# Performance work log

Hardware: AMD Instinct MI355X
Metric: run time of the kernel (lower is better)

Reference implementation:

```python
import jax, jax.numpy as jnp
import numpy as np
import math

EMBED = 1024
HEADS = 16
HEAD_DIM = EMBED // HEADS
B, S = 2, 2048


def setup_inputs() -> dict:
    key = jax.random.key(0)
    ks = jax.random.split(key, 12)
    sc = 1.0 / math.sqrt(EMBED)
    inp = {
        'query': jax.random.normal(ks[0], (B, S, EMBED), jnp.float32),
        'key': jax.random.normal(ks[1], (B, S, EMBED), jnp.float32),
        'values': jax.random.normal(ks[2], (B, S, EMBED), jnp.float32),
        # causal mask, broadcastable to [B, H, S, S]; masked where == 0
        'mask': jnp.tril(jnp.ones((S, S), jnp.int32))[None, None, :, :],
        'Wq': jax.random.normal(ks[3], (EMBED, EMBED), jnp.float32) * sc,
        'bq': jnp.zeros((EMBED,), jnp.float32),
        'Wk': jax.random.normal(ks[4], (EMBED, EMBED), jnp.float32) * sc,
        'bk': jnp.zeros((EMBED,), jnp.float32),
        'Wv': jax.random.normal(ks[5], (EMBED, EMBED), jnp.float32) * sc,
        'bv': jnp.zeros((EMBED,), jnp.float32),
        'Wo': jax.random.normal(ks[6], (EMBED, EMBED), jnp.float32) * sc,
        'bo': jnp.zeros((EMBED,), jnp.float32),
    }
    return inp


def reference(query, key, values, mask, Wq, bq, Wk, bk, Wv, bv, Wo, bo):
    # linear projections (torch Linear: x @ W.T + b)
    q = query @ Wq.T + bq
    k = key @ Wk.T + bk
    v = values @ Wv.T + bv
    b, sq, _ = q.shape
    sk = k.shape[1]
    q = q.reshape(b, sq, HEADS, HEAD_DIM)  # bqhd
    k = k.reshape(b, sk, HEADS, HEAD_DIM)  # bkhd
    v = v.reshape(b, sk, HEADS, HEAD_DIM)  # bkhd
    energy = jnp.einsum('bqhd,bkhd->bhqk', q, k) / math.sqrt(HEAD_DIM)
    energy = jnp.where(mask == 0, jnp.float32(-1e10), energy)
    attn = jax.nn.softmax(energy, axis=-1)
    out = jnp.einsum('bhqk,bkhd->bqhd', attn, v).reshape(b, sq, EMBED)
    return out @ Wo.T + bo
```

## Files before the change

### kernel.cpp

```cpp
#include <hip/hip_runtime.h>

typedef unsigned short u16;
typedef unsigned int   u32;
typedef __attribute__((ext_vector_type(4))) float f32x4;
typedef __attribute__((ext_vector_type(8))) short bf16x8;
typedef __attribute__((ext_vector_type(4))) u32   u32x4;
typedef __attribute__((ext_vector_type(4))) u16   u16x4;

#define AS1 __attribute__((address_space(1)))
#define AS3 __attribute__((address_space(3)))

__device__ __forceinline__ u16 f2bf(float f) {
  union { float f; u32 u; } v; v.f = f;
  u32 r = v.u + 0x7FFFu + ((v.u >> 16) & 1u);
  return (u16)(r >> 16);
}

__device__ __forceinline__ void g2l16(const void* g, void* l) {
  __builtin_amdgcn_global_load_lds((const AS1 u32*)g, (AS3 u32*)l, 16, 0, 0);
}

struct CvtArgs {
  const float* src[7];
  u16*         dst[7];
  int          n4[7];
};

__global__ __launch_bounds__(256) void cvt_kernel(CvtArgs a) {
  const int ai = blockIdx.y;
  const f32x4* s = (const f32x4*)a.src[ai];
  u16x4*       d = (u16x4*)a.dst[ai];
  const int n4 = a.n4[ai];
  for (int i = blockIdx.x * 256 + threadIdx.x; i < n4; i += gridDim.x * 256) {
    f32x4 v = s[i];
    u16x4 o;
    o[0] = f2bf(v[0]); o[1] = f2bf(v[1]); o[2] = f2bf(v[2]); o[3] = f2bf(v[3]);
    d[i] = o;
  }
}

template <typename OutT, int TM>
__device__ __forceinline__ void gemm_core(
    const u16* __restrict__ A, const u16* __restrict__ W,
    const float* __restrict__ bias, bool rowbias,
    OutT* __restrict__ C, int ldc, int row0, int col0,
    u16* sA, u16* sB, int tid)
{
  constexpr int K = 1024;
  constexpr int MF = TM / 32;
  const int lane = tid & 63, wid = tid >> 6;
  const int l15 = lane & 15, hi = lane >> 4;
  const int wr = (wid >> 1) * (TM / 2), wc = (wid & 1) * 64;

  f32x4 acc[MF][4];
#pragma unroll
  for (int i = 0; i < MF; ++i)
#pragma unroll
    for (int j = 0; j < 4; ++j) acc[i][j] = f32x4{0.f, 0.f, 0.f, 0.f};

  auto stage = [&](int kt) {
#pragma unroll
    for (int it = 0; it < TM / 64; ++it) {
      int idx = it * 256 + tid;
      int r = idx >> 2, g = idx & 3;
      int gs = g ^ ((r >> 1) & 3);
      g2l16(A + (size_t)(row0 + r) * K + kt * 32 + gs * 8, sA + idx * 8);
    }
#pragma unroll
    for (int it = 0; it < 2; ++it) {
      int idx = it * 256 + tid;
      int r = idx >> 2, g = idx & 3;
      int gs = g ^ ((r >> 1) & 3);
      g2l16(W + (size_t)(col0 + r) * K + kt * 32 + gs * 8, sB + idx * 8);
    }
  };

  stage(0);
  for (int kt = 0; kt < K / 32; ++kt) {
    __syncthreads();
    bf16x8 aF[MF], bF[4];
#pragma unroll
    for (int mf = 0; mf < MF; ++mf) {
      int r = wr + mf * 16 + l15;
      int g = hi ^ ((r >> 1) & 3);
      aF[mf] = *(const bf16x8*)(sA + r * 32 + g * 8);
    }
#pragma unroll
    for (int nf = 0; nf < 4; ++nf) {
      int r = wc + nf * 16 + l15;
      int g = hi ^ ((r >> 1) & 3);
      bF[nf] = *(const bf16x8*)(sB + r * 32 + g * 8);
    }
#pragma unroll
    for (int mf = 0; mf < MF; ++mf)
#pragma unroll
      for (int nf = 0; nf < 4; ++nf)
        acc[mf][nf] = __builtin_amdgcn_mfma_f32_16x16x32_bf16(aF[mf], bF[nf], acc[mf][nf], 0, 0, 0);
    __syncthreads();
    if (kt + 1 < K / 32) stage(kt + 1);
  }

#pragma unroll
  for (int nf = 0; nf < 4; ++nf) {
    int gcol = col0 + wc + nf * 16 + l15;
    float bcol = rowbias ? 0.f : bias[gcol];
#pragma unroll
    for (int mf = 0; mf < MF; ++mf) {
#pragma unroll
      for (int r = 0; r < 4; ++r) {
        int grow = row0 + wr + mf * 16 + hi * 4 + r;
        float bv = rowbias ? bias[grow] : bcol;
        float v = acc[mf][nf][r] + bv;
        if constexpr (sizeof(OutT) == 2) {
          ((u16*)C)[(size_t)grow * ldc + gcol] = f2bf(v);
        } else {
          ((float*)C)[(size_t)grow * ldc + gcol] = v;
        }
      }
    }
  }
}

struct ProjArgs {
  const u16* A[3]; const u16* W[3]; const float* bias[3];
  u16* C[3];
};

__global__ __launch_bounds__(256, 2) void gemm_proj(ProjArgs p) {
  __shared__ alignas(16) u16 sA[128 * 32];
  __shared__ alignas(16) u16 sB[128 * 32];
  const int bid = blockIdx.x;
  int which, row0, col0, ldc;
  bool rowbias;
  if (bid < 512) {
    which = bid >> 8;
    int l = bid & 255;
    col0 = (l & 7) << 7;
    row0 = (l >> 3) << 7;
    ldc = 1024; rowbias = false;
  } else {
    which = 2;
    int l = bid - 512;
    col0 = (l & 31) << 7;
    row0 = (l >> 5) << 7;
    ldc = 4096; rowbias = true;
  }
  gemm_core<u16, 128>(p.A[which], p.W[which], p.bias[which], rowbias,
                      p.C[which], ldc, row0, col0, sA, sB, threadIdx.x);
}

__global__ __launch_bounds__(256, 2) void gemm_out(
    const u16* __restrict__ A, const u16* __restrict__ W,
    const float* __restrict__ bias, float* __restrict__ C)
{
  __shared__ alignas(16) u16 sA[64 * 32];
  __shared__ alignas(16) u16 sB[128 * 32];
  const int bid = blockIdx.x;
  const int col0 = (bid & 7) << 7;
  const int row0 = (bid >> 3) << 6;
  gemm_core<float, 64>(A, W, bias, false, C, 1024, row0, col0, sA, sB, threadIdx.x);
}

__global__ __launch_bounds__(256, 4) void attn_fwd(
    const u16* __restrict__ Q, const u16* __restrict__ Kg, const u16* __restrict__ VT,
    u16* __restrict__ ctx)
{
  __shared__ alignas(16) u16 sK[2][64 * 64];
  __shared__ alignas(16) u16 sVt[2][64 * 64];
  __shared__ alignas(16) u16 sP[4][16 * 64];

  const int tid = threadIdx.x;
  const int lane = tid & 63, wid = tid >> 6;
  const int l15 = lane & 15, hi = lane >> 4;

  const int wg = blockIdx.x;
  const int jj = wg >> 5, bh = wg & 31;
  const int rr = jj >> 3, kk = jj & 7;
  int xt;
  if (rr == 0)      xt = 31 - kk;
  else if (rr == 1) xt = 16 + kk;
  else if (rr == 2) xt = 15 - kk;
  else              xt = kk;

  const int b = bh >> 4, h = bh & 15;
  const int q0 = xt * 64;
  const int q0w = q0 + wid * 16;
  const size_t base  = ((size_t)b * 2048) * 1024 + h * 64;
  const size_t vbase = (size_t)(h * 64) * 4096 + b * 2048;

  bf16x8 qf[2];
#pragma unroll
  for (int kh = 0; kh < 2; ++kh)
    qf[kh] = *(const bf16x8*)(Q + base + (size_t)(q0w + l15) * 1024 + kh * 32 + hi * 8);

  f32x4 o[4];
  float lS[4];
#pragma unroll
  for (int nf = 0; nf < 4; ++nf) o[nf] = f32x4{0.f, 0.f, 0.f, 0.f};
#pragma unroll
  for (int r = 0; r < 4; ++r) lS[r] = 0.f;

  u16* sPw = &sP[wid][0];
  const int nt = xt + 1;

  auto issueK = [&](int ti, int bb) {
#pragma unroll
    for (int it = 0; it < 2; ++it) {
      int idx = it * 256 + tid;
      int r = idx >> 3, g = idx & 7;
      int gs = g ^ (r & 7);
      g2l16(Kg + base + (size_t)(ti * 64 + r) * 1024 + gs * 8, &sK[bb][idx * 8]);
    }
  };
  auto issueV = [&](int ti, int bb) {
#pragma unroll
    for (int it = 0; it < 2; ++it) {
      int idx = it * 256 + tid;
      int r = idx >> 3, g = idx & 7;
      int gs = g ^ (r & 7);
      g2l16(VT + vbase + (size_t)r * 4096 + ti * 64 + gs * 8, &sVt[bb][idx * 8]);
    }
  };

  issueK(0, 0);
  issueV(0, 0);
  __syncthreads();

  constexpr float SCL = 0.125f * 1.44269504f;

  for (int ti = 0; ti < nt; ++ti) {
    const int cur = ti & 1;
    const bool pf = (ti + 1 < nt);
    if (pf) {
      issueK(ti + 1, cur ^ 1);
      issueV(ti + 1, cur ^ 1);
    }

    const int kv0 = ti * 64;
    const bool needmask = (ti == xt);
    const u16* sKc = &sK[cur][0];
    const u16* sVc = &sVt[cur][0];

    f32x4 s[4];
#pragma unroll
    for (int n = 0; n < 4; ++n) s[n] = f32x4{0.f, 0.f, 0.f, 0.f};
#pragma unroll
    for (int n = 0; n < 4; ++n) {
      int kvr = n * 16 + l15;
      bf16x8 kf0 = *(const bf16x8*)(sKc + kvr * 64 + ((hi) ^ (kvr & 7)) * 8);
      bf16x8 kf1 = *(const bf16x8*)(sKc + kvr * 64 + ((4 + hi) ^ (kvr & 7)) * 8);
      s[n] = __builtin_amdgcn_mfma_f32_16x16x32_bf16(qf[0], kf0, s[n], 0, 0, 0);
      s[n] = __builtin_amdgcn_mfma_f32_16x16x32_bf16(qf[1], kf1, s[n], 0, 0, 0);
    }

#pragma unroll
    for (int r = 0; r < 4; ++r) {
      float lsum = 0.f;
#pragma unroll
      for (int n = 0; n < 4; ++n) {
        float sv = s[n][r] * SCL;
        if (needmask) {
          int qa = q0w + hi * 4 + r;
          int ka = kv0 + n * 16 + l15;
          if (ka > qa) sv = -1e30f;
        }
        float p = __builtin_amdgcn_exp2f(sv);
        s[n][r] = p;
        lsum += p;
      }
      lS[r] += lsum;
    }

#pragma unroll
    for (int n = 0; n < 4; ++n) {
      int c = n * 16 + l15;
#pragma unroll
      for (int r = 0; r < 4; ++r) {
        int q = hi * 4 + r;
        sPw[q * 64 + (c ^ ((q & 7) << 3))] = f2bf(s[n][r]);
      }
    }

#pragma unroll
    for (int kq = 0; kq < 2; ++kq) {
      bf16x8 pa, vb[4];
      pa = *(const bf16x8*)(sPw + l15 * 64 + ((kq * 32 + hi * 8) ^ ((l15 & 7) << 3)));
#pragma unroll
      for (int nf = 0; nf < 4; ++nf) {
        int rd = nf * 16 + l15;
        vb[nf] = *(const bf16x8*)(sVc + rd * 64 + ((kq * 4 + hi) ^ (rd & 7)) * 8);
      }
#pragma unroll
      for (int nf = 0; nf < 4; ++nf)
        o[nf] = __builtin_amdgcn_mfma_f32_16x16x32_bf16(pa, vb[nf], o[nf], 0, 0, 0);
    }

    __syncthreads();
  }

#pragma unroll
  for (int r = 0; r < 4; ++r) {
    float t = lS[r];
    t += __shfl_xor(t, 1);
    t += __shfl_xor(t, 2);
    t += __shfl_xor(t, 4);
    t += __shfl_xor(t, 8);
    float inv = 1.f / t;
    size_t rowoff = base + (size_t)(q0w + hi * 4 + r) * 1024;
#pragma unroll
    for (int nf = 0; nf < 4; ++nf)
      ctx[rowoff + nf * 16 + l15] = f2bf(o[nf][r] * inv);
  }
}

extern "C" void kernel_launch(void* const* d_in, const int* in_sizes, int n_in,
                              void* d_out, int out_size, void* d_ws, size_t ws_size,
                              hipStream_t stream) {
  const float* query = (const float*)d_in[0];
  const float* key   = (const float*)d_in[1];
  const float* vals  = (const float*)d_in[2];
  const float* Wq = (const float*)d_in[4];
  const float* bq = (const float*)d_in[5];
  const float* Wk = (const float*)d_in[6];
  const float* bk = (const float*)d_in[7];
  const float* Wv = (const float*)d_in[8];
  const float* bv = (const float*)d_in[9];
  const float* Wo = (const float*)d_in[10];
  const float* bo = (const float*)d_in[11];
  float* out = (float*)d_out;

  if (ws_size < 58720256) return;

  u16* ws = (u16*)d_ws;
  u16* xq = ws + 0;
  u16* xk = ws + 4194304;
  u16* xv = ws + 8388608;
  u16* wq = ws + 12582912;
  u16* wk = ws + 13631488;
  u16* wv = ws + 14680064;
  u16* wo = ws + 15728640;
  u16* Qb = ws + 16777216;
  u16* Kb = ws + 20971520;
  u16* VT = ws + 25165824;
  u16* ctx = xq;

  CvtArgs ca;
  ca.src[0] = query; ca.dst[0] = xq; ca.n4[0] = 1048576;
  ca.src[1] = key;   ca.dst[1] = xk; ca.n4[1] = 1048576;
  ca.src[2] = vals;  ca.dst[2] = xv; ca.n4[2] = 1048576;
  ca.src[3] = Wq;    ca.dst[3] = wq; ca.n4[3] = 262144;
  ca.src[4] = Wk;    ca.dst[4] = wk; ca.n4[4] = 262144;
  ca.src[5] = Wv;    ca.dst[5] = wv; ca.n4[5] = 262144;
  ca.src[6] = Wo;    ca.dst[6] = wo; ca.n4[6] = 262144;
  cvt_kernel<<<dim3(256, 7), 256, 0, stream>>>(ca);

  ProjArgs pa;
  pa.A[0] = xq; pa.W[0] = wq; pa.bias[0] = bq; pa.C[0] = Qb;
  pa.A[1] = xk; pa.W[1] = wk; pa.bias[1] = bk; pa.C[1] = Kb;
  pa.A[2] = wv; pa.W[2] = xv; pa.bias[2] = bv; pa.C[2] = VT;
  gemm_proj<<<dim3(768), 256, 0, stream>>>(pa);

  attn_fwd<<<dim3(1024), 256, 0, stream>>>(Qb, Kb, VT, ctx);

  gemm_out<<<dim3(512), 256, 0, stream>>>(ctx, wo, bo, out);
}
```

Before: 119.8 us.

## Double GEMM K-tile to 64, remap blocks across XCDs, truncate P to bf16

The GEMM core now stages 64-wide K tiles instead of 32, which halves the number of barrier-separated iterations. It uses an 8-way XOR swizzle and issues the next tile's global-to-LDS loads before the MFMAs of the current tile, so loads overlap compute. Block indices in the projection and output GEMMs are permuted so that consecutive tiles land on the same XCD for better L2 reuse. The softmax probabilities are converted to bf16 by truncation rather than round-to-nearest, which saves ALU work but adds a small rounding bias. LDS use per block doubles, which may limit occupancy.

```diff
diff --git a/kernel.cpp b/kernel.cpp
--- a/kernel.cpp
+++ b/kernel.cpp
@@ -2,10 +2,10 @@
 
 typedef unsigned short u16;
 typedef unsigned int   u32;
-typedef __attribute__((ext_vector_type(4))) float f32x4;
-typedef __attribute__((ext_vector_type(8))) short bf16x8;
-typedef __attribute__((ext_vector_type(4))) u32   u32x4;
-typedef __attribute__((ext_vector_type(4))) u16   u16x4;
+typedef __attribute__((ext_vector_type(4)))  float f32x4;
+typedef __attribute__((ext_vector_type(8)))  short bf16x8;
+typedef __attribute__((ext_vector_type(4)))  u32   u32x4;
+typedef __attribute__((ext_vector_type(4)))  u16   u16x4;
 
 #define AS1 __attribute__((address_space(1)))
 #define AS3 __attribute__((address_space(3)))
@@ -14,6 +14,11 @@
   union { float f; u32 u; } v; v.f = f;
   u32 r = v.u + 0x7FFFu + ((v.u >> 16) & 1u);
   return (u16)(r >> 16);
+}
+
+__device__ __forceinline__ u16 f2bf_t(float f) {
+  union { float f; u32 u; } v; v.f = f;
+  return (u16)(v.u >> 16);
 }
 
 __device__ __forceinline__ void g2l16(const void* g, void* l) {
@@ -40,7 +45,7 @@
 }
 
 template <typename OutT, int TM>
-__device__ __forceinline__ void gemm_core(
+__device__ __forceinline__ void gemm_core64(
     const u16* __restrict__ A, const u16* __restrict__ W,
     const float* __restrict__ bias, bool rowbias,
     OutT* __restrict__ C, int ldc, int row0, int col0,
@@ -60,44 +65,48 @@
 
   auto stage = [&](int kt) {
 #pragma unroll
-    for (int it = 0; it < TM / 64; ++it) {
+    for (int it = 0; it < TM / 32; ++it) {
       int idx = it * 256 + tid;
-      int r = idx >> 2, g = idx & 3;
-      int gs = g ^ ((r >> 1) & 3);
-      g2l16(A + (size_t)(row0 + r) * K + kt * 32 + gs * 8, sA + idx * 8);
-    }
-#pragma unroll
-    for (int it = 0; it < 2; ++it) {
+      int r = idx >> 3, g = idx & 7;
+      int gs = g ^ (r & 7);
+      g2l16(A + (size_t)(row0 + r) * K + kt * 64 + gs * 8, sA + idx * 8);
+    }
+#pragma unroll
+    for (int it = 0; it < 4; ++it) {
       int idx = it * 256 + tid;
-      int r = idx >> 2, g = idx & 3;
-      int gs = g ^ ((r >> 1) & 3);
-      g2l16(W + (size_t)(col0 + r) * K + kt * 32 + gs * 8, sB + idx * 8);
+      int r = idx >> 3, g = idx & 7;
+      int gs = g ^ (r & 7);
+      g2l16(W + (size_t)(col0 + r) * K + kt * 64 + gs * 8, sB + idx * 8);
     }
   };
 
   stage(0);
-  for (int kt = 0; kt < K / 32; ++kt) {
+  for (int kt = 0; kt < K / 64; ++kt) {
     __syncthreads();
-    bf16x8 aF[MF], bF[4];
+    bf16x8 aF[MF][2], bF[4][2];
 #pragma unroll
     for (int mf = 0; mf < MF; ++mf) {
       int r = wr + mf * 16 + l15;
-      int g = hi ^ ((r >> 1) & 3);
-      aF[mf] = *(const bf16x8*)(sA + r * 32 + g * 8);
+#pragma unroll
+      for (int kh = 0; kh < 2; ++kh)
+        aF[mf][kh] = *(const bf16x8*)(sA + r * 64 + ((kh * 4 + hi) ^ (r & 7)) * 8);
     }
 #pragma unroll
     for (int nf = 0; nf < 4; ++nf) {
       int r = wc + nf * 16 + l15;
-      int g = hi ^ ((r >> 1) & 3);
-      bF[nf] = *(const bf16x8*)(sB + r * 32 + g * 8);
-    }
-#pragma unroll
-    for (int mf = 0; mf < MF; ++mf)
-#pragma unroll
-      for (int nf = 0; nf < 4; ++nf)
-        acc[mf][nf] = __builtin_amdgcn_mfma_f32_16x16x32_bf16(aF[mf], bF[nf], acc[mf][nf], 0, 0, 0);
+#pragma unroll
+      for (int kh = 0; kh < 2; ++kh)
+        bF[nf][kh] = *(const bf16x8*)(sB + r * 64 + ((kh * 4 + hi) ^ (r & 7)) * 8);
+    }
     __syncthreads();
-    if (kt + 1 < K / 32) stage(kt + 1);
+    if (kt + 1 < K / 64) stage(kt + 1);
+#pragma unroll
+    for (int kh = 0; kh < 2; ++kh)
+#pragma unroll
+      for (int mf = 0; mf < MF; ++mf)
+#pragma unroll
+        for (int nf = 0; nf < 4; ++nf)
+          acc[mf][nf] = __builtin_amdgcn_mfma_f32_16x16x32_bf16(aF[mf][kh], bF[nf][kh], acc[mf][nf], 0, 0, 0);
   }
 
 #pragma unroll
@@ -127,38 +136,38 @@
 };
 
 __global__ __launch_bounds__(256, 2) void gemm_proj(ProjArgs p) {
-  __shared__ alignas(16) u16 sA[128 * 32];
-  __shared__ alignas(16) u16 sB[128 * 32];
-  const int bid = blockIdx.x;
+  __shared__ alignas(16) u16 sA[128 * 64];
+  __shared__ alignas(16) u16 sB[128 * 64];
+  const int w = (blockIdx.x & 7) * 96 + (blockIdx.x >> 3);
   int which, row0, col0, ldc;
   bool rowbias;
-  if (bid < 512) {
-    which = bid >> 8;
-    int l = bid & 255;
+  if (w < 512) {
+    which = w >> 8;
+    int l = w & 255;
     col0 = (l & 7) << 7;
     row0 = (l >> 3) << 7;
     ldc = 1024; rowbias = false;
   } else {
     which = 2;
-    int l = bid - 512;
+    int l = w - 512;
     col0 = (l & 31) << 7;
     row0 = (l >> 5) << 7;
     ldc = 4096; rowbias = true;
   }
-  gemm_core<u16, 128>(p.A[which], p.W[which], p.bias[which], rowbias,
-                      p.C[which], ldc, row0, col0, sA, sB, threadIdx.x);
+  gemm_core64<u16, 128>(p.A[which], p.W[which], p.bias[which], rowbias,
+                        p.C[which], ldc, row0, col0, sA, sB, threadIdx.x);
 }
 
 __global__ __launch_bounds__(256, 2) void gemm_out(
     const u16* __restrict__ A, const u16* __restrict__ W,
     const float* __restrict__ bias, float* __restrict__ C)
 {
-  __shared__ alignas(16) u16 sA[64 * 32];
-  __shared__ alignas(16) u16 sB[128 * 32];
-  const int bid = blockIdx.x;
-  const int col0 = (bid & 7) << 7;
-  const int row0 = (bid >> 3) << 6;
-  gemm_core<float, 64>(A, W, bias, false, C, 1024, row0, col0, sA, sB, threadIdx.x);
+  __shared__ alignas(16) u16 sA[64 * 64];
+  __shared__ alignas(16) u16 sB[128 * 64];
+  const int w = (blockIdx.x & 7) * 64 + (blockIdx.x >> 3);
+  const int col0 = (w & 7) << 7;
+  const int row0 = (w >> 3) << 6;
+  gemm_core64<float, 64>(A, W, bias, false, C, 1024, row0, col0, sA, sB, threadIdx.x);
 }
 
 __global__ __launch_bounds__(256, 4) void attn_fwd(
@@ -277,7 +286,7 @@
 #pragma unroll
       for (int r = 0; r < 4; ++r) {
         int q = hi * 4 + r;
-        sPw[q * 64 + (c ^ ((q & 7) << 3))] = f2bf(s[n][r]);
+        sPw[q * 64 + (c ^ ((q & 7) << 3))] = f2bf_t(s[n][r]);
       }
     }
 
```

After: 106.8 us. 10.9% less time.
